# Performance work log

Hardware: AMD Instinct MI355X
Metric: run time of the kernel (lower is better)

Reference implementation:

```python
import jax, jax.numpy as jnp
import numpy as np

N_C = 50000
N_N = 50000
E = 500000
D = 128


def _graph_conv(x_src, src, dst, n_src, n_dst, W, b):
    # DGL GraphConv, norm='both': symmetric degree normalization, then linear.
    ones = jnp.ones(src.shape, x_src.dtype)
    deg_out = jax.ops.segment_sum(ones, src, num_segments=n_src)
    deg_in = jax.ops.segment_sum(ones, dst, num_segments=n_dst)
    norm_src = jnp.maximum(deg_out, 1.0) ** -0.5  # [n_src]
    norm_dst = jnp.maximum(deg_in, 1.0) ** -0.5   # [n_dst]
    m = (x_src * norm_src[:, None])[src]          # [E, D] gather
    agg = jax.ops.segment_sum(m, dst, num_segments=n_dst)  # [n_dst, D]
    return (agg * norm_dst[:, None]) @ W + b


def _sage_conv(x_src, x_dst, src, dst, n_dst, W_self, W_neigh, b):
    # DGL SAGEConv, aggregator='mean': fc_self(h_dst) + fc_neigh(mean_neigh) + bias.
    ones = jnp.ones(src.shape, x_src.dtype)
    deg_in = jnp.maximum(jax.ops.segment_sum(ones, dst, num_segments=n_dst), 1.0)
    h_neigh = jax.ops.segment_sum(x_src[src], dst, num_segments=n_dst) / deg_in[:, None]
    return x_dst @ W_self + h_neigh @ W_neigh + b


def setup_inputs() -> dict:
    key = jax.random.key(0)
    ks = jax.random.split(key, 20)
    s = 1.0 / np.sqrt(D)
    inp = {
        'feat_C': jax.random.normal(ks[0], (N_C, D), jnp.float32),
        'feat_N': jax.random.normal(ks[1], (N_N, D), jnp.float32),
        'W1_cc': jax.random.normal(ks[2], (D, D), jnp.float32) * s,
        'b1_cc': jnp.zeros((D,), jnp.float32),
        'W1_cn': jax.random.normal(ks[3], (D, D), jnp.float32) * s,
        'b1_cn': jnp.zeros((D,), jnp.float32),
        'W1_self': jax.random.normal(ks[4], (D, D), jnp.float32) * s,
        'W1_neigh': jax.random.normal(ks[5], (D, D), jnp.float32) * s,
        'b1_nn': jnp.zeros((D,), jnp.float32),
        'W2_cc': jax.random.normal(ks[6], (D, D), jnp.float32) * s,
        'b2_cc': jnp.zeros((D,), jnp.float32),
        'W2_cn': jax.random.normal(ks[7], (D, D), jnp.float32) * s,
        'b2_cn': jnp.zeros((D,), jnp.float32),
        'W2_self': jax.random.normal(ks[8], (D, D), jnp.float32) * s,
        'W2_neigh': jax.random.normal(ks[9], (D, D), jnp.float32) * s,
        'b2_nn': jnp.zeros((D,), jnp.float32),
        'cc_src': jax.random.randint(ks[10], (E,), 0, N_C),
        'cc_dst': jax.random.randint(ks[11], (E,), 0, N_C),
        'cn_src': jax.random.randint(ks[12], (E,), 0, N_C),
        'cn_dst': jax.random.randint(ks[13], (E,), 0, N_N),
        'nn_src': jax.random.randint(ks[14], (E,), 0, N_N),
        'nn_dst': jax.random.randint(ks[15], (E,), 0, N_N),
    }
    return inp


def reference(feat_C, feat_N, W1_cc, b1_cc, W1_cn, b1_cn, W1_self, W1_neigh, b1_nn,
              W2_cc, b2_cc, W2_cn, b2_cn, W2_self, W2_neigh, b2_nn,
              cc_src, cc_dst, cn_src, cn_dst, nn_src, nn_dst):
    # layer 1 (HeteroGraphConv, aggregate='sum') + relu
    hC = _graph_conv(feat_C, cc_src, cc_dst, N_C, N_C, W1_cc, b1_cc)
    hN = (_graph_conv(feat_C, cn_src, cn_dst, N_C, N_N, W1_cn, b1_cn)
          + _sage_conv(feat_N, feat_N, nn_src, nn_dst, N_N, W1_self, W1_neigh, b1_nn))
    hC = jax.nn.relu(hC)
    hN = jax.nn.relu(hN)
    # layer 2
    oC = _graph_conv(hC, cc_src, cc_dst, N_C, N_C, W2_cc, b2_cc)
    oN = (_graph_conv(hC, cn_src, cn_dst, N_C, N_N, W2_cn, b2_cn)
          + _sage_conv(hN, hN, nn_src, nn_dst, N_N, W2_self, W2_neigh, b2_nn))
    return oC, oN
```

## Files before the change

### kernel.cpp

```cpp
#include <hip/hip_runtime.h>

#define NCN 50000
#define NE  500000
#define DF  128

#define BSHIFT 9
#define NBUCK 98
#define BK 128
#define CAP 7168
#define CHUNK 4096

typedef __attribute__((ext_vector_type(8))) short mfrag;
typedef __attribute__((ext_vector_type(4))) float facc4;

__device__ inline ushort f2bf(float x) {
    unsigned u = __float_as_uint(x);
    unsigned r = (u + 0x7FFFu + ((u >> 16) & 1u)) >> 16;
    return (ushort)r;
}
__device__ inline float bf2f(ushort h) { return __uint_as_float(((unsigned)h) << 16); }

__device__ inline void store_split4m(ushort* __restrict__ T, int row, int lane4,
                                     float4 v, int mode) {
    ushort h0 = f2bf(v.x); ushort l0 = f2bf(v.x - bf2f(h0));
    ushort h1 = f2bf(v.y); ushort l1 = f2bf(v.y - bf2f(h1));
    ushort h2 = f2bf(v.z); ushort l2 = f2bf(v.z - bf2f(h2));
    ushort h3 = f2bf(v.w); ushort l3 = f2bf(v.w - bf2f(h3));
    uint2 hp = make_uint2((uint)h0 | ((uint)h1 << 16), (uint)h2 | ((uint)h3 << 16));
    uint2 lp = make_uint2((uint)l0 | ((uint)l1 << 16), (uint)l2 | ((uint)l3 << 16));
    size_t hiOff, loOff;
    if (mode == 0) { hiOff = (size_t)row * DF; loOff = (size_t)NCN * DF + (size_t)row * DF; }
    else           { hiOff = (size_t)row * 256; loOff = hiOff + 128; }
    *(uint2*)(T + hiOff + lane4 * 4) = hp;
    *(uint2*)(T + loOff + lane4 * 4) = lp;
}

__global__ __launch_bounds__(256) void hist2_k(
    const int* __restrict__ cc_src, const int* __restrict__ cn_src,
    int* __restrict__ cnt2)
{
    int i = blockIdx.x * 256 + threadIdx.x;
    if (i >= NE) return;
    atomicAdd(&cnt2[cc_src[i]], 1);
    atomicAdd(&cnt2[NCN + cn_src[i]], 1);
}

__global__ __launch_bounds__(256) void srcnorm_k(
    const int* __restrict__ cnt2, float* __restrict__ snorm2, int n2)
{
    int i = blockIdx.x * 256 + threadIdx.x;
    if (i >= n2) return;
    int c = cnt2[i]; if (c < 1) c = 1;
    snorm2[i] = rsqrtf((float)c);
}

__global__ __launch_bounds__(256) void binA_k(
    const int* __restrict__ cc_src, const int* __restrict__ cc_dst,
    const int* __restrict__ cn_src, const int* __restrict__ cn_dst,
    const int* __restrict__ nn_src, const int* __restrict__ nn_dst,
    uint2* __restrict__ R, int* __restrict__ bc)
{
    const int s = blockIdx.y;
    const int* key; const int* pay;
    switch (s) {
      case 0: key = cc_dst; pay = cc_src; break;
      case 1: key = cn_dst; pay = cn_src; break;
      default: key = nn_dst; pay = nn_src; break;
    }
    __shared__ uint2 rec[CHUNK];
    __shared__ int lhist[BK], lofs[BK], lcur[BK], gbase[BK];
    __shared__ int ls[256];
    const int tid = threadIdx.x;
    const int base = blockIdx.x * CHUNK;

    int k[16], p[16];
    #pragma unroll
    for (int j = 0; j < 16; ++j) {
        int e = base + j * 256 + tid;
        bool valid = (e < NE);
        k[j] = valid ? key[e] : -1;
        p[j] = valid ? pay[e] : 0;
    }
    if (tid < BK) lhist[tid] = 0;
    __syncthreads();
    #pragma unroll
    for (int j = 0; j < 16; ++j)
        if (k[j] >= 0) atomicAdd(&lhist[k[j] >> BSHIFT], 1);
    __syncthreads();
    int v = (tid < BK) ? lhist[tid] : 0;
    ls[tid] = v;
    __syncthreads();
    #pragma unroll
    for (int off = 1; off < 128; off <<= 1) {
        int t = (tid >= off) ? ls[tid - off] : 0;
        __syncthreads();
        ls[tid] += t;
        __syncthreads();
    }
    if (tid < BK) { int e = ls[tid] - v; lofs[tid] = e; lcur[tid] = e; }
    __syncthreads();
    #pragma unroll
    for (int j = 0; j < 16; ++j) {
        if (k[j] >= 0) {
            int b = k[j] >> BSHIFT;
            int pos = atomicAdd(&lcur[b], 1);
            rec[pos] = make_uint2((unsigned)k[j], (unsigned)p[j]);
        }
    }
    __syncthreads();
    if (tid < BK) {
        int c = lcur[tid] - lofs[tid];
        gbase[tid] = (c > 0) ? atomicAdd(&bc[s * BK + tid], c) : 0;
    }
    __syncthreads();
    int total = ls[127];
    for (int i = tid; i < total; i += 256) {
        uint2 r = rec[i];
        int b = (int)(r.x >> BSHIFT);
        int gi = gbase[b] + (i - lofs[b]);
        R[((size_t)s * NBUCK + b) * CAP + gi] = r;
    }
}

__global__ __launch_bounds__(256) void binB_k(
    const uint2* __restrict__ R, const int* __restrict__ bc,
    int* __restrict__ rp3, int* __restrict__ col3)
{
    const int b = blockIdx.x;
    const int s = blockIdx.y;
    const int tid = threadIdx.x;
    __shared__ int cnt[512];
    __shared__ int lofs[512];
    __shared__ int ls[256];
    __shared__ int sbase;

    const int nrec = bc[s * BK + b];
    const uint2* rec = R + ((size_t)s * NBUCK + b) * CAP;

    for (int i = tid; i < 512; i += 256) cnt[i] = 0;
    __syncthreads();
    for (int i = tid; i < nrec; i += 256)
        atomicAdd(&cnt[rec[i].x & 511], 1);
    __syncthreads();

    {
        int v = (tid < b) ? bc[s * BK + tid] : 0;
        ls[tid] = v;
        __syncthreads();
        for (int off = 128; off > 0; off >>= 1) {
            if (tid < off) ls[tid] += ls[tid + off];
            __syncthreads();
        }
        if (tid == 0) sbase = ls[0];
        __syncthreads();
    }
    const int colBase = sbase;

    int v0 = cnt[2 * tid], v1 = cnt[2 * tid + 1];
    int pairSum = v0 + v1;
    ls[tid] = pairSum;
    __syncthreads();
    #pragma unroll
    for (int off = 1; off < 256; off <<= 1) {
        int t = (tid >= off) ? ls[tid - off] : 0;
        __syncthreads();
        ls[tid] += t;
        __syncthreads();
    }
    int excl = ls[tid] - pairSum;
    lofs[2 * tid] = excl;
    lofs[2 * tid + 1] = excl + v0;
    __syncthreads();
    const int total = ls[255];

    int* rp = rp3 + (size_t)s * (NCN + 1);
    for (int j = tid; j < 512; j += 256) {
        int d = b * 512 + j;
        if (d < NCN) rp[d] = colBase + lofs[j];
    }
    if (b == NBUCK - 1 && tid == 0) rp[NCN] = colBase + total;
    __syncthreads();

    int* col = col3 + (size_t)s * NE + colBase;
    for (int i = tid; i < nrec; i += 256) {
        uint2 r = rec[i];
        int pos = atomicAdd(&lofs[r.x & 511], 1);
        col[pos] = (int)r.y;
    }
}

__global__ __launch_bounds__(256) void wconv_k(
    const float* __restrict__ Wm0, const float* __restrict__ Wm1,
    const float* __restrict__ Wm2, const float* __restrict__ Wm3,
    const float* __restrict__ Wm4, const float* __restrict__ Wm5,
    const float* __restrict__ Wm6, const float* __restrict__ Wm7,
    ushort* __restrict__ out)
{
    const float* Ws[8] = {Wm0, Wm1, Wm2, Wm3, Wm4, Wm5, Wm6, Wm7};
    const float* W = Ws[blockIdx.x];
    ushort* o = out + (size_t)blockIdx.x * 32768;
    for (int i = threadIdx.x; i < 16384; i += 256) {
        int c = i >> 13;
        int r = i & 8191;
        int n = r >> 6;
        int jj = r & 63;
        int kk = c * 64 + (jj ^ ((n & 7) << 3));
        float wv = W[kk * 128 + n];
        ushort h = f2bf(wv);
        float lv = wv - bf2f(h);
        o[c * 16384 + r] = h;
        o[c * 16384 + 8192 + r] = f2bf(lv);
    }
}

__global__ __launch_bounds__(256) void agg_k(
    const float* __restrict__ X0, const int* __restrict__ rp0,
    const int* __restrict__ col0, const float* __restrict__ sc0,
    ushort* __restrict__ out0, int m0,
    const float* __restrict__ X1, const int* __restrict__ rp1,
    const int* __restrict__ col1, const float* __restrict__ sc1,
    ushort* __restrict__ out1, int m1,
    const float* __restrict__ X2, const int* __restrict__ rp2,
    const int* __restrict__ col2, const float* __restrict__ sc2,
    ushort* __restrict__ out2, int m2)
{
    const float* X; const int* rp; const int* col; const float* sc; ushort* out; int mode;
    if (blockIdx.y == 0)      { X = X0; rp = rp0; col = col0; sc = sc0; out = out0; mode = m0; }
    else if (blockIdx.y == 1) { X = X1; rp = rp1; col = col1; sc = sc1; out = out1; mode = m1; }
    else                      { X = X2; rp = rp2; col = col2; sc = sc2; out = out2; mode = m2; }

    int wid = (blockIdx.x * 256 + threadIdx.x) >> 6;
    int half = (threadIdx.x >> 5) & 1;
    int lane4 = threadIdx.x & 31;
    int row = wid * 2 + half;
    if (row >= NCN) return;
    int e0 = rp[row], e1 = rp[row + 1];
    const bool useSc = (sc != nullptr);
    float4 a = make_float4(0.f, 0.f, 0.f, 0.f);
    int e = e0;
    while (e < e1) {
        int cnt = e1 - e; if (cnt > 32) cnt = 32;
        int myc = (lane4 < cnt) ? col[e + lane4] : 0;
        float mysc = (useSc && lane4 < cnt) ? sc[myc] : 1.0f;
        int j = 0;
        for (; j + 4 <= cnt; j += 4) {
            int s0 = __shfl(myc, j, 32),     s1 = __shfl(myc, j + 1, 32);
            int s2 = __shfl(myc, j + 2, 32), s3 = __shfl(myc, j + 3, 32);
            float c0 = __shfl(mysc, j, 32),     c1 = __shfl(mysc, j + 1, 32);
            float c2 = __shfl(mysc, j + 2, 32), c3 = __shfl(mysc, j + 3, 32);
            const float4 u0 = *(const float4*)(X + (size_t)s0 * DF + lane4 * 4);
            const float4 u1 = *(const float4*)(X + (size_t)s1 * DF + lane4 * 4);
            const float4 u2 = *(const float4*)(X + (size_t)s2 * DF + lane4 * 4);
            const float4 u3 = *(const float4*)(X + (size_t)s3 * DF + lane4 * 4);
            a.x = fmaf(u0.x, c0, a.x); a.y = fmaf(u0.y, c0, a.y);
            a.z = fmaf(u0.z, c0, a.z); a.w = fmaf(u0.w, c0, a.w);
            a.x = fmaf(u1.x, c1, a.x); a.y = fmaf(u1.y, c1, a.y);
            a.z = fmaf(u1.z, c1, a.z); a.w = fmaf(u1.w, c1, a.w);
            a.x = fmaf(u2.x, c2, a.x); a.y = fmaf(u2.y, c2, a.y);
            a.z = fmaf(u2.z, c2, a.z); a.w = fmaf(u2.w, c2, a.w);
            a.x = fmaf(u3.x, c3, a.x); a.y = fmaf(u3.y, c3, a.y);
            a.z = fmaf(u3.z, c3, a.z); a.w = fmaf(u3.w, c3, a.w);
        }
        for (; j < cnt; ++j) {
            int s0 = __shfl(myc, j, 32);
            float c0 = __shfl(mysc, j, 32);
            const float4 u0 = *(const float4*)(X + (size_t)s0 * DF + lane4 * 4);
            a.x = fmaf(u0.x, c0, a.x); a.y = fmaf(u0.y, c0, a.y);
            a.z = fmaf(u0.z, c0, a.z); a.w = fmaf(u0.w, c0, a.w);
        }
        e += cnt;
    }
    int deg = e1 - e0; if (deg < 1) deg = 1;
    float dsc = useSc ? rsqrtf((float)deg) : (1.0f / (float)deg);
    a.x *= dsc; a.y *= dsc; a.z *= dsc; a.w *= dsc;
    store_split4m(out, row, lane4, a, mode);
}

template<int NSRC, bool RELU, int F32S, bool A1INT>
__device__ __forceinline__ void gemm_body(
    ushort* __restrict__ Wsm,
    const void* __restrict__ A0, const void* __restrict__ A1, const void* __restrict__ A2,
    const ushort* __restrict__ Wi0, const ushort* __restrict__ Wi1, const ushort* __restrict__ Wi2,
    const float* __restrict__ b0, const float* __restrict__ b1,
    float* __restrict__ Y)
{
    constexpr int NCH = 2 * NSRC;
    const int tid = threadIdx.x;
    const int l = tid & 63;
    const int wv = tid >> 6;
    const int wvr = wv & 1;
    const int wvc = wv >> 1;
    const int r0 = blockIdx.x * 128;
    const int M = NCN;

    const void*   Aarr[3] = {A0, A1, A2};
    const ushort* Warr[3] = {Wi0, Wi1, Wi2};

    int arow[4];
    #pragma unroll
    for (int rt = 0; rt < 4; ++rt) {
        int r = r0 + wvr * 64 + rt * 16 + (l & 15);
        arow[rt] = (r < M) ? r : (M - 1);
    }
    const int kgrp = (l >> 4) * 8;

    facc4 acc[4][4];
    #pragma unroll
    for (int rt = 0; rt < 4; ++rt)
        #pragma unroll
        for (int ct = 0; ct < 4; ++ct)
            acc[rt][ct] = (facc4){0.f, 0.f, 0.f, 0.f};

    uint4 Wr[8];
    auto loadWr = [&](int c) {
        int s = c >> 1, chalf = c & 1;
        const uint4* wp = (const uint4*)(Warr[s] + chalf * 16384);
        #pragma unroll
        for (int i = 0; i < 8; ++i) Wr[i] = wp[i * 256 + tid];
    };

    mfrag ahA[4], alA[4], ahB[4], alB[4];
    auto loadA = [&](int c, int ks, mfrag (&ah)[4], mfrag (&al)[4]) {
        int s = c >> 1;
        int k0 = (c & 1) * 64 + ks * 32;
        if (s == F32S) {
            const float* F = (const float*)Aarr[s];
            #pragma unroll
            for (int rt = 0; rt < 4; ++rt) {
                const float* p = F + (size_t)arow[rt] * DF + k0 + kgrp;
                float4 v0 = *(const float4*)p;
                float4 v1 = *(const float4*)(p + 4);
                union { mfrag m; ushort u[8]; } H, L;
                float vv0[4] = {v0.x, v0.y, v0.z, v0.w};
                float vv1[4] = {v1.x, v1.y, v1.z, v1.w};
                #pragma unroll
                for (int j = 0; j < 4; ++j) {
                    ushort h = f2bf(vv0[j]);
                    H.u[j] = h; L.u[j] = f2bf(vv0[j] - bf2f(h));
                }
                #pragma unroll
                for (int j = 0; j < 4; ++j) {
                    ushort h = f2bf(vv1[j]);
                    H.u[4 + j] = h; L.u[4 + j] = f2bf(vv1[j] - bf2f(h));
                }
                ah[rt] = H.m; al[rt] = L.m;
            }
        } else {
            const ushort* T = (const ushort*)Aarr[s];
            const bool INT = (s == 1 && A1INT);
            const int rs = INT ? 256 : DF;
            const size_t lo = INT ? 128 : (size_t)NCN * DF;
            #pragma unroll
            for (int rt = 0; rt < 4; ++rt) {
                size_t o = (size_t)arow[rt] * rs + k0 + kgrp;
                ah[rt] = *(const mfrag*)(T + o);
                al[rt] = *(const mfrag*)(T + o + lo);
            }
        }
    };

    auto compute = [&](int ks, const mfrag (&ah)[4], const mfrag (&al)[4]) {
        const int kbyte = ks * 64 + (l >> 4) * 16;
        #pragma unroll
        for (int ct = 0; ct < 4; ++ct) {
            int colc = wvc * 64 + ct * 16 + (l & 15);
            int widx = colc * 64 + ((kbyte ^ ((colc & 7) << 4)) >> 1);
            mfrag w_hi = *(const mfrag*)(Wsm + widx);
            mfrag w_lo = *(const mfrag*)(Wsm + 8192 + widx);
            #pragma unroll
            for (int rt = 0; rt < 4; ++rt) {
                acc[rt][ct] = __builtin_amdgcn_mfma_f32_16x16x32_bf16(ah[rt], w_hi, acc[rt][ct], 0, 0, 0);
                acc[rt][ct] = __builtin_amdgcn_mfma_f32_16x16x32_bf16(ah[rt], w_lo, acc[rt][ct], 0, 0, 0);
                acc[rt][ct] = __builtin_amdgcn_mfma_f32_16x16x32_bf16(al[rt], w_hi, acc[rt][ct], 0, 0, 0);
            }
        }
    };

    loadWr(0);
    #pragma unroll
    for (int c = 0; c < NCH; ++c) {
        __syncthreads();
        {
            uint4* wd = (uint4*)Wsm;
            #pragma unroll
            for (int i = 0; i < 8; ++i) wd[i * 256 + tid] = Wr[i];
        }
        loadA(c, 0, ahA, alA);
        if (c + 1 < NCH) loadWr(c + 1);
        __syncthreads();
        loadA(c, 1, ahB, alB);
        compute(0, ahA, alA);
        compute(1, ahB, alB);
    }
    __syncthreads();

    float bias[4];
    #pragma unroll
    for (int ct = 0; ct < 4; ++ct) {
        int colc = wvc * 64 + ct * 16 + (l & 15);
        float bv = b0 ? b0[colc] : 0.f;
        if (b1) bv += b1[colc];
        bias[ct] = bv;
    }
    #pragma unroll
    for (int rt = 0; rt < 4; ++rt) {
        #pragma unroll
        for (int q = 0; q < 4; ++q) {
            int row = r0 + wvr * 64 + rt * 16 + (l >> 4) * 4 + q;
            if (row < M) {
                #pragma unroll
                for (int ct = 0; ct < 4; ++ct) {
                    float v = acc[rt][ct][q] + bias[ct];
                    if (RELU) v = fmaxf(v, 0.f);
                    Y[(size_t)row * DF + wvc * 64 + ct * 16 + (l & 15)] = v;
                }
            }
        }
    }
}

template<bool RELU, bool A1INT>
__global__ __launch_bounds__(256, 2) void fgemm2_k(
    const ushort* __restrict__ AN0, const ushort* __restrict__ AN1,
    const float* __restrict__ AN2f,
    const ushort* __restrict__ WiN0, const ushort* __restrict__ WiN1,
    const ushort* __restrict__ WiN2,
    const float* __restrict__ bN0, const float* __restrict__ bN1,
    float* __restrict__ YN,
    const ushort* __restrict__ AC0, const ushort* __restrict__ WiC,
    const float* __restrict__ bC, float* __restrict__ YC)
{
    __shared__ ushort Wsm[16384];
    if (blockIdx.z == 0)
        gemm_body<3, RELU, 2, A1INT>(Wsm, AN0, AN1, AN2f, WiN0, WiN1, WiN2,
                                     bN0, bN1, YN);
    else
        gemm_body<1, RELU, -1, false>(Wsm, AC0, nullptr, nullptr,
                                      WiC, nullptr, nullptr, bC, nullptr, YC);
}

template<bool RELU>
__global__ __launch_bounds__(256, 2) void gemmN_k(
    const ushort* __restrict__ A0, const ushort* __restrict__ A1i,
    const float* __restrict__ A2f,
    const ushort* __restrict__ Wi0, const ushort* __restrict__ Wi1,
    const ushort* __restrict__ Wi2,
    const float* __restrict__ b0, const float* __restrict__ b1,
    float* __restrict__ Y)
{
    __shared__ ushort Wsm[16384];
    gemm_body<3, RELU, 2, true>(Wsm, A0, A1i, A2f, Wi0, Wi1, Wi2, b0, b1, Y);
}

template<bool RELU>
__global__ __launch_bounds__(256, 2) void gemmC_k(
    const ushort* __restrict__ A0, const ushort* __restrict__ Wi0,
    const float* __restrict__ b0, float* __restrict__ Y)
{
    __shared__ ushort Wsm[16384];
    gemm_body<1, RELU, -1, false>(Wsm, A0, nullptr, nullptr, Wi0, nullptr, nullptr,
                                  b0, nullptr, Y);
}

extern "C" void kernel_launch(void* const* d_in, const int* in_sizes, int n_in,
                              void* d_out, int out_size, void* d_ws, size_t ws_size,
                              hipStream_t stream)
{
    (void)in_sizes; (void)n_in; (void)out_size;
    const float* feat_C   = (const float*)d_in[0];
    const float* feat_N   = (const float*)d_in[1];
    const float* W1_cc    = (const float*)d_in[2];
    const float* b1_cc    = (const float*)d_in[3];
    const float* W1_cn    = (const float*)d_in[4];
    const float* b1_cn    = (const float*)d_in[5];
    const float* W1_self  = (const float*)d_in[6];
    const float* W1_neigh = (const float*)d_in[7];
    const float* b1_nn    = (const float*)d_in[8];
    const float* W2_cc    = (const float*)d_in[9];
    const float* b2_cc    = (const float*)d_in[10];
    const float* W2_cn    = (const float*)d_in[11];
    const float* b2_cn    = (const float*)d_in[12];
    const float* W2_self  = (const float*)d_in[13];
    const float* W2_neigh = (const float*)d_in[14];
    const float* b2_nn    = (const float*)d_in[15];
    const int* cc_src = (const int*)d_in[16];
    const int* cc_dst = (const int*)d_in[17];
    const int* cn_src = (const int*)d_in[18];
    const int* cn_dst = (const int*)d_in[19];
    const int* nn_src = (const int*)d_in[20];
    const int* nn_dst = (const int*)d_in[21];

    char* ws = (char*)d_ws;
    size_t off = 0;
    auto take = [&](size_t bytes) -> char* {
        char* p = ws + off;
        off = (off + bytes + 255) & ~(size_t)255;
        return p;
    };
    const size_t TBL = (size_t)2 * NCN * DF * sizeof(ushort);
    int*    rp3    = (int*)take((size_t)3 * (NCN + 1) * sizeof(int));
    int*    col3   = (int*)take((size_t)3 * NE * sizeof(int));
    float*  snorm2 = (float*)take((size_t)2 * NCN * sizeof(float));
    int*    cnt2   = (int*)take((size_t)2 * NCN * sizeof(int));
    int*    bc     = (int*)take((size_t)3 * BK * sizeof(int));
    ushort* Wimg   = (ushort*)take((size_t)8 * 32768 * sizeof(ushort));
    char* bigRegion = take(2 * TBL);
    uint2*  R  = (uint2*)bigRegion;
    ushort* P0 = (ushort*)bigRegion;
    ushort* P1 = (ushort*)(bigRegion + TBL);
    const bool useP2 = (ws_size >= off + TBL);
    ushort* P2 = useP2 ? (ushort*)take(TBL) : nullptr;

    float* oC = (float*)d_out;
    float* oN = oC + (size_t)NCN * DF;
    ushort* oC_us = (ushort*)oC;
    ushort* oN_us = (ushort*)oN;

    const int edgeBlocks = (NE + 255) / 256;
    const int binABlocks = (NE + CHUNK - 1) / CHUNK;
    const int aggBlocks  = (((NCN + 1) / 2) * 64 + 255) / 256;
    const int gemmBlocks = (NCN + 127) / 128;

    auto img = [&](int m) { return (const ushort*)(Wimg + (size_t)m * 32768); };
    const int* rpCC = rp3 + 0 * (NCN + 1);
    const int* rpCN = rp3 + 1 * (NCN + 1);
    const int* rpNN = rp3 + 2 * (NCN + 1);
    const int* colCC = col3 + 0 * NE;
    const int* colCN = col3 + 1 * NE;
    const int* colNN = col3 + 2 * NE;
    const float* snCC = snorm2 + 0 * NCN;
    const float* snCN = snorm2 + 1 * NCN;

    hipMemsetAsync(cnt2, 0, (size_t)2 * NCN * sizeof(int), stream);
    hipMemsetAsync(bc, 0, (size_t)3 * BK * sizeof(int), stream);
    hist2_k<<<edgeBlocks, 256, 0, stream>>>(cc_src, cn_src, cnt2);
    srcnorm_k<<<(2 * NCN + 255) / 256, 256, 0, stream>>>(cnt2, snorm2, 2 * NCN);
    binA_k<<<dim3(binABlocks, 3), 256, 0, stream>>>(cc_src, cc_dst, cn_src, cn_dst,
                                                    nn_src, nn_dst, R, bc);
    binB_k<<<dim3(NBUCK, 3), 256, 0, stream>>>(R, bc, rp3, col3);
    wconv_k<<<8, 256, 0, stream>>>(W1_cc, W1_cn, W1_neigh, W1_self,
                                   W2_cc, W2_cn, W2_neigh, W2_self, Wimg);

    if (useP2) {
        agg_k<<<dim3(aggBlocks, 3), 256, 0, stream>>>(
            feat_C, rpCC, colCC, snCC, P0, 0,
            feat_C, rpCN, colCN, snCN, P1, 0,
            feat_N, rpNN, colNN, nullptr, P2, 0);
        fgemm2_k<true, false><<<dim3(gemmBlocks, 1, 2), 256, 0, stream>>>(
            P1, P2, feat_N, img(1), img(2), img(3), b1_cn, b1_nn, oN,
            P0, img(0), b1_cc, oC);
        agg_k<<<dim3(aggBlocks, 3), 256, 0, stream>>>(
            oC, rpCC, colCC, snCC, P0, 0,
            oC, rpCN, colCN, snCN, P1, 0,
            oN, rpNN, colNN, nullptr, P2, 0);
        fgemm2_k<false, false><<<dim3(gemmBlocks, 1, 2), 256, 0, stream>>>(
            P1, P2, oN, img(5), img(6), img(7), b2_cn, b2_nn, oN,
            P0, img(4), b2_cc, oC);
    } else {
        agg_k<<<dim3(aggBlocks, 3), 256, 0, stream>>>(
            feat_C, rpCC, colCC, snCC, P0, 0,
            feat_C, rpCN, colCN, snCN, P1, 0,
            feat_N, rpNN, colNN, nullptr, oN_us, 1);
        fgemm2_k<true, true><<<dim3(gemmBlocks, 1, 2), 256, 0, stream>>>(
            P1, oN_us, feat_N, img(1), img(2), img(3), b1_cn, b1_nn, oN,
            P0, img(0), b1_cc, oC);
        agg_k<<<dim3(aggBlocks, 2), 256, 0, stream>>>(
            oC, rpCC, colCC, snCC, P0, 0,
            oC, rpCN, colCN, snCN, P1, 0,
            nullptr, nullptr, nullptr, nullptr, nullptr, 0);
        agg_k<<<dim3(aggBlocks, 1), 256, 0, stream>>>(
            oN, rpNN, colNN, nullptr, oC_us, 1,
            nullptr, nullptr, nullptr, nullptr, nullptr, 0,
            nullptr, nullptr, nullptr, nullptr, nullptr, 0);
        gemmN_k<false><<<gemmBlocks, 256, 0, stream>>>(P1, oC_us, oN,
                                                       img(5), img(6), img(7),
                                                       b2_cn, b2_nn, oN);
        gemmC_k<false><<<gemmBlocks, 256, 0, stream>>>(P0, img(4), b2_cc, oC);
    }
}
```

Before: 435.9 us.

## Fold source-degree histogram into binning and widen GEMM blocks to 512 threads

Removes the separate hist2_k edge pass by counting source degrees inside binA_k, which already loads src/dst indices, so one kernel launch and one read of the index arrays go away. The GEMM body is restructured so each 512-thread block covers 256 rows and stages a whole 128x128 weight image (hi+lo) in 64KB LDS at once. A full source then needs one staging step instead of two half-chunks, with more sync-free K steps and A loads interleaved with MFMAs. The cost is higher LDS use per block, which may limit occupancy, and a changed wave-to-tile mapping.

```diff
diff --git a/kernel.cpp b/kernel.cpp
--- a/kernel.cpp
+++ b/kernel.cpp
@@ -35,16 +35,6 @@
     *(uint2*)(T + loOff + lane4 * 4) = lp;
 }
 
-__global__ __launch_bounds__(256) void hist2_k(
-    const int* __restrict__ cc_src, const int* __restrict__ cn_src,
-    int* __restrict__ cnt2)
-{
-    int i = blockIdx.x * 256 + threadIdx.x;
-    if (i >= NE) return;
-    atomicAdd(&cnt2[cc_src[i]], 1);
-    atomicAdd(&cnt2[NCN + cn_src[i]], 1);
-}
-
 __global__ __launch_bounds__(256) void srcnorm_k(
     const int* __restrict__ cnt2, float* __restrict__ snorm2, int n2)
 {
@@ -58,7 +48,7 @@
     const int* __restrict__ cc_src, const int* __restrict__ cc_dst,
     const int* __restrict__ cn_src, const int* __restrict__ cn_dst,
     const int* __restrict__ nn_src, const int* __restrict__ nn_dst,
-    uint2* __restrict__ R, int* __restrict__ bc)
+    uint2* __restrict__ R, int* __restrict__ bc, int* __restrict__ cnt2)
 {
     const int s = blockIdx.y;
     const int* key; const int* pay;
@@ -80,6 +70,12 @@
         bool valid = (e < NE);
         k[j] = valid ? key[e] : -1;
         p[j] = valid ? pay[e] : 0;
+    }
+    if (s < 2) {
+        int* cn = cnt2 + (size_t)s * NCN;
+        #pragma unroll
+        for (int j = 0; j < 16; ++j)
+            if (k[j] >= 0) atomicAdd(&cn[p[j]], 1);
     }
     if (tid < BK) lhist[tid] = 0;
     __syncthreads();
@@ -284,13 +280,12 @@
     const float* __restrict__ b0, const float* __restrict__ b1,
     float* __restrict__ Y)
 {
-    constexpr int NCH = 2 * NSRC;
     const int tid = threadIdx.x;
     const int l = tid & 63;
     const int wv = tid >> 6;
-    const int wvr = wv & 1;
-    const int wvc = wv >> 1;
-    const int r0 = blockIdx.x * 128;
+    const int wvr = wv >> 1;
+    const int wvc = wv & 1;
+    const int r0 = blockIdx.x * 256;
     const int M = NCN;
 
     const void*   Aarr[3] = {A0, A1, A2};
@@ -312,17 +307,15 @@
             acc[rt][ct] = (facc4){0.f, 0.f, 0.f, 0.f};
 
     uint4 Wr[8];
-    auto loadWr = [&](int c) {
-        int s = c >> 1, chalf = c & 1;
-        const uint4* wp = (const uint4*)(Warr[s] + chalf * 16384);
+    auto loadWr = [&](int s) {
+        const uint4* wp = (const uint4*)Warr[s];
         #pragma unroll
-        for (int i = 0; i < 8; ++i) Wr[i] = wp[i * 256 + tid];
+        for (int i = 0; i < 8; ++i) Wr[i] = wp[i * 512 + tid];
     };
 
     mfrag ahA[4], alA[4], ahB[4], alB[4];
-    auto loadA = [&](int c, int ks, mfrag (&ah)[4], mfrag (&al)[4]) {
-        int s = c >> 1;
-        int k0 = (c & 1) * 64 + ks * 32;
+    auto loadA = [&](int s, int ks, mfrag (&ah)[4], mfrag (&al)[4]) {
+        const int k0 = ks * 32;
         if (s == F32S) {
             const float* F = (const float*)Aarr[s];
             #pragma unroll
@@ -360,13 +353,14 @@
     };
 
     auto compute = [&](int ks, const mfrag (&ah)[4], const mfrag (&al)[4]) {
-        const int kbyte = ks * 64 + (l >> 4) * 16;
+        const int cb = (ks >> 1) * 16384;
+        const int kbyte = (ks & 1) * 64 + (l >> 4) * 16;
         #pragma unroll
         for (int ct = 0; ct < 4; ++ct) {
             int colc = wvc * 64 + ct * 16 + (l & 15);
-            int widx = colc * 64 + ((kbyte ^ ((colc & 7) << 4)) >> 1);
+            int widx = cb + colc * 64 + ((kbyte ^ ((colc & 7) << 4)) >> 1);
             mfrag w_hi = *(const mfrag*)(Wsm + widx);
-            mfrag w_lo = *(const mfrag*)(Wsm + 8192 + widx);
+            mfrag w_lo = *(const mfrag*)(Wsm + widx + 8192);
             #pragma unroll
             for (int rt = 0; rt < 4; ++rt) {
                 acc[rt][ct] = __builtin_amdgcn_mfma_f32_16x16x32_bf16(ah[rt], w_hi, acc[rt][ct], 0, 0, 0);
@@ -378,19 +372,23 @@
 
     loadWr(0);
     #pragma unroll
-    for (int c = 0; c < NCH; ++c) {
-        __syncthreads();
+    for (int s = 0; s < NSRC; ++s) {
+        __syncthreads();
+        loadA(s, 0, ahA, alA);
         {
             uint4* wd = (uint4*)Wsm;
             #pragma unroll
-            for (int i = 0; i < 8; ++i) wd[i * 256 + tid] = Wr[i];
-        }
-        loadA(c, 0, ahA, alA);
-        if (c + 1 < NCH) loadWr(c + 1);
-        __syncthreads();
-        loadA(c, 1, ahB, alB);
+            for (int i = 0; i < 8; ++i) wd[i * 512 + tid] = Wr[i];
+        }
+        if (s + 1 < NSRC) loadWr(s + 1);
+        __syncthreads();
+        loadA(s, 1, ahB, alB);
         compute(0, ahA, alA);
+        loadA(s, 2, ahA, alA);
         compute(1, ahB, alB);
+        loadA(s, 3, ahB, alB);
+        compute(2, ahA, alA);
+        compute(3, ahB, alB);
     }
     __syncthreads();
 
@@ -420,7 +418,7 @@
 }
 
 template<bool RELU, bool A1INT>
-__global__ __launch_bounds__(256, 2) void fgemm2_k(
+__global__ __launch_bounds__(512, 4) void fgemm2_k(
     const ushort* __restrict__ AN0, const ushort* __restrict__ AN1,
     const float* __restrict__ AN2f,
     const ushort* __restrict__ WiN0, const ushort* __restrict__ WiN1,
@@ -430,7 +428,7 @@
     const ushort* __restrict__ AC0, const ushort* __restrict__ WiC,
     const float* __restrict__ bC, float* __restrict__ YC)
 {
-    __shared__ ushort Wsm[16384];
+    __shared__ ushort Wsm[32768];
     if (blockIdx.z == 0)
         gemm_body<3, RELU, 2, A1INT>(Wsm, AN0, AN1, AN2f, WiN0, WiN1, WiN2,
                                      bN0, bN1, YN);
@@ -440,7 +438,7 @@
 }
 
 template<bool RELU>
-__global__ __launch_bounds__(256, 2) void gemmN_k(
+__global__ __launch_bounds__(512, 4) void gemmN_k(
     const ushort* __restrict__ A0, const ushort* __restrict__ A1i,
     const float* __restrict__ A2f,
     const ushort* __restrict__ Wi0, const ushort* __restrict__ Wi1,
@@ -448,16 +446,16 @@
     const float* __restrict__ b0, const float* __restrict__ b1,
     float* __restrict__ Y)
 {
-    __shared__ ushort Wsm[16384];
+    __shared__ ushort Wsm[32768];
     gemm_body<3, RELU, 2, true>(Wsm, A0, A1i, A2f, Wi0, Wi1, Wi2, b0, b1, Y);
 }
 
 template<bool RELU>
-__global__ __launch_bounds__(256, 2) void gemmC_k(
+__global__ __launch_bounds__(512, 4) void gemmC_k(
     const ushort* __restrict__ A0, const ushort* __restrict__ Wi0,
     const float* __restrict__ b0, float* __restrict__ Y)
 {
-    __shared__ ushort Wsm[16384];
+    __shared__ ushort Wsm[32768];
     gemm_body<1, RELU, -1, false>(Wsm, A0, nullptr, nullptr, Wi0, nullptr, nullptr,
                                   b0, nullptr, Y);
 }
@@ -516,10 +514,9 @@
     ushort* oC_us = (ushort*)oC;
     ushort* oN_us = (ushort*)oN;
 
-    const int edgeBlocks = (NE + 255) / 256;
     const int binABlocks = (NE + CHUNK - 1) / CHUNK;
     const int aggBlocks  = (((NCN + 1) / 2) * 64 + 255) / 256;
-    const int gemmBlocks = (NCN + 127) / 128;
+    const int gemmBlocks = (NCN + 255) / 256;
 
     auto img = [&](int m) { return (const ushort*)(Wimg + (size_t)m * 32768); };
     const int* rpCC = rp3 + 0 * (NCN + 1);
@@ -533,10 +530,9 @@
 
     hipMemsetAsync(cnt2, 0, (size_t)2 * NCN * sizeof(int), stream);
     hipMemsetAsync(bc, 0, (size_t)3 * BK * sizeof(int), stream);
-    hist2_k<<<edgeBlocks, 256, 0, stream>>>(cc_src, cn_src, cnt2);
+    binA_k<<<dim3(binABlocks, 3), 256, 0, stream>>>(cc_src, cc_dst, cn_src, cn_dst,
+                                                    nn_src, nn_dst, R, bc, cnt2);
     srcnorm_k<<<(2 * NCN + 255) / 256, 256, 0, stream>>>(cnt2, snorm2, 2 * NCN);
-    binA_k<<<dim3(binABlocks, 3), 256, 0, stream>>>(cc_src, cc_dst, cn_src, cn_dst,
-                                                    nn_src, nn_dst, R, bc);
     binB_k<<<dim3(NBUCK, 3), 256, 0, stream>>>(R, bc, rp3, col3);
     wconv_k<<<8, 256, 0, stream>>>(W1_cc, W1_cn, W1_neigh, W1_self,
                                    W2_cc, W2_cn, W2_neigh, W2_self, Wimg);
@@ -546,14 +542,14 @@
             feat_C, rpCC, colCC, snCC, P0, 0,
             feat_C, rpCN, colCN, snCN, P1, 0,
             feat_N, rpNN, colNN, nullptr, P2, 0);
-        fgemm2_k<true, false><<<dim3(gemmBlocks, 1, 2), 256, 0, stream>>>(
+        fgemm2_k<true, false><<<dim3(gemmBlocks, 1, 2), 512, 0, stream>>>(
             P1, P2, feat_N, img(1), img(2), img(3), b1_cn, b1_nn, oN,
             P0, img(0), b1_cc, oC);
         agg_k<<<dim3(aggBlocks, 3), 256, 0, stream>>>(
             oC, rpCC, colCC, snCC, P0, 0,
             oC, rpCN, colCN, snCN, P1, 0,
             oN, rpNN, colNN, nullptr, P2, 0);
-        fgemm2_k<false, false><<<dim3(gemmBlocks, 1, 2), 256, 0, stream>>>(
+        fgemm2_k<false, false><<<dim3(gemmBlocks, 1, 2), 512, 0, stream>>>(
             P1, P2, oN, img(5), img(6), img(7), b2_cn, b2_nn, oN,
             P0, img(4), b2_cc, oC);
     } else {
@@ -561,7 +557,7 @@
             feat_C, rpCC, colCC, snCC, P0, 0,
             feat_C, rpCN, colCN, snCN, P1, 0,
             feat_N, rpNN, colNN, nullptr, oN_us, 1);
-        fgemm2_k<true, true><<<dim3(gemmBlocks, 1, 2), 256, 0, stream>>>(
+        fgemm2_k<true, true><<<dim3(gemmBlocks, 1, 2), 512, 0, stream>>>(
             P1, oN_us, feat_N, img(1), img(2), img(3), b1_cn, b1_nn, oN,
             P0, img(0), b1_cc, oC);
         agg_k<<<dim3(aggBlocks, 2), 256, 0, stream>>>(
@@ -572,9 +568,9 @@
             oN, rpNN, colNN, nullptr, oC_us, 1,
             nullptr, nullptr, nullptr, nullptr, nullptr, 0,
             nullptr, nullptr, nullptr, nullptr, nullptr, 0);
-        gemmN_k<false><<<gemmBlocks, 256, 0, stream>>>(P1, oC_us, oN,
+        gemmN_k<false><<<gemmBlocks, 512, 0, stream>>>(P1, oC_us, oN,
                                                        img(5), img(6), img(7),
                                                        b2_cn, b2_nn, oN);
-        gemmC_k<false><<<gemmBlocks, 256, 0, stream>>>(P0, img(4), b2_cc, oC);
-    }
-}
+        gemmC_k<false><<<gemmBlocks, 512, 0, stream>>>(P0, img(4), b2_cc, oC);
+    }
+}
```

Measured after the change: 506.2 us. +16.1%, slower.
